# Kernel optimization log

Hardware: AMD Instinct MI355X
Metric: run time of the kernel (lower is better)

## Reference

```python
import jax, jax.numpy as jnp
import numpy as np

B, N, CIN, K = 4, 4096, 64, 16
MLP = [64, 64, 128]
EPS = 1e-5


def setup_inputs() -> dict:
    key = jax.random.key(0)
    ks = jax.random.split(key, 8)
    inp = {
        "xyz": jax.random.normal(ks[0], (B, N, 3), dtype=jnp.float32),
        "points": jax.random.normal(ks[1], (B, N, CIN), dtype=jnp.float32),
    }
    last = 3 + CIN
    for i, oc in enumerate(MLP):
        inp[f"w{i}"] = jax.random.normal(ks[2 + i], (oc, last), dtype=jnp.float32) * 0.05
        inp[f"b{i}"] = jnp.zeros((oc,), dtype=jnp.float32)
        inp[f"g{i}"] = jnp.ones((oc,), dtype=jnp.float32)
        inp[f"be{i}"] = jnp.zeros((oc,), dtype=jnp.float32)
        inp[f"rm{i}"] = jnp.zeros((oc,), dtype=jnp.float32)
        inp[f"rv{i}"] = jnp.ones((oc,), dtype=jnp.float32)
        last = oc
    return inp


def reference(xyz, points, w0, b0, g0, be0, rm0, rv0,
              w1, b1, g1, be1, rm1, rv1,
              w2, b2, g2, be2, rm2, rv2):
    # knn via squared pairwise distance (same argsort order as cdist)
    sq = jnp.sum(xyz * xyz, axis=-1)  # (B,N)
    d2 = sq[:, :, None] + sq[:, None, :] - 2.0 * jnp.einsum('bnc,bmc->bnm', xyz, xyz)
    _, idx = jax.lax.top_k(-d2, K)  # (B,N,K), smallest-distance neighbors

    bidx = jnp.arange(xyz.shape[0])[:, None, None]  # (B,1,1)
    grouped_xyz = xyz[bidx, idx] - xyz[:, :, None, :]     # (B,N,K,3) relative coords
    grouped_pts = points[bidx, idx]                        # (B,N,K,CIN)
    h = jnp.concatenate([grouped_xyz, grouped_pts], axis=-1)  # (B,N,K,3+CIN)

    layers = [(w0, b0, g0, be0, rm0, rv0),
              (w1, b1, g1, be1, rm1, rv1),
              (w2, b2, g2, be2, rm2, rv2)]
    for (w, b, g, be, rm, rv) in layers:
        # 1x1 conv == per-point linear; BN in eval mode (running stats)
        h = jnp.einsum('bnkc,oc->bnko', h, w) + b
        h = (h - rm) * jax.lax.rsqrt(rv + EPS) * g + be
        h = jax.nn.relu(h)
    new_points = jnp.max(h, axis=2)  # max over K neighbors -> (B,N,C_out)
    return new_points
```

## Files before the change

kernel.cpp:

```cpp
#include <hip/hip_runtime.h>

#define NPT   4096
#define KNN_K 16
#define EPSV  1e-5f

#define W1T_OFF 4352
#define B1_OFF  8448
#define W2T_OFF 8512
#define B2_OFF  16704
#define IDX_OFF 16832
#define P_OFF   344512
#define Q_OFF   1393088

typedef unsigned long long ull;

__device__ __forceinline__ ull minu64(ull a, ull b) { return a < b ? a : b; }
__device__ __forceinline__ ull maxu64(ull a, ull b) { return a > b ? a : b; }

__device__ __forceinline__ ull bitonic_sort64(ull v, int lane) {
#pragma unroll
  for (int k = 2; k <= 64; k <<= 1) {
#pragma unroll
    for (int j = k >> 1; j > 0; j >>= 1) {
      ull o = __shfl_xor(v, j);
      bool lower = (lane & j) == 0;
      bool up = (lane & k) == 0;
      v = (lower == up) ? minu64(v, o) : maxu64(v, o);
    }
  }
  return v;
}

__device__ __forceinline__ ull bitonic_merge64(ull v, int lane) {
#pragma unroll
  for (int j = 32; j > 0; j >>= 1) {
    ull o = __shfl_xor(v, j);
    v = ((lane & j) == 0) ? minu64(v, o) : maxu64(v, o);
  }
  return v;
}

__global__ __launch_bounds__(256) void mega_kernel(
    const float* __restrict__ xyz, const float* __restrict__ points,
    const float* __restrict__ w0, const float* __restrict__ b0, const float* __restrict__ g0,
    const float* __restrict__ be0, const float* __restrict__ rm0, const float* __restrict__ rv0,
    const float* __restrict__ w1, const float* __restrict__ b1, const float* __restrict__ g1,
    const float* __restrict__ be1, const float* __restrict__ rm1, const float* __restrict__ rv1,
    const float* __restrict__ w2, const float* __restrict__ b2, const float* __restrict__ g2,
    const float* __restrict__ be2, const float* __restrict__ rm2, const float* __restrict__ rv2,
    float* __restrict__ ws, int* __restrict__ knnOut) {
  __shared__ __align__(16) unsigned char smem[20480];
  int blk = blockIdx.x;
  int tid = threadIdx.x;

  if (blk < 4096) {
    float4* tile = (float4*)smem;
    ull* buf = (ull*)(smem + 16384);
    int lane = tid & 63, w = tid >> 6;
    int b = blk >> 10;
    int n = ((blk & 1023) << 2) + w;
    const float* xb = xyz + (size_t)b * NPT * 3;

    float4 q;
    {
      const float* qp = xb + n * 3;
      float qx = qp[0], qy = qp[1], qz = qp[2];
      float qsq = __fadd_rn(__fadd_rn(__fmul_rn(qx, qx), __fmul_rn(qy, qy)),
                            __fmul_rn(qz, qz));
      q = make_float4(qx, qy, qz, qsq);
    }
    ull R = ~0ull;
    ull thresh = ~0ull;
    int cnt = 0;
    ull ltmask = (lane == 0) ? 0ull : (~0ull >> (64 - lane));
    const float4* r4 = (const float4*)xb;

#pragma unroll 1
    for (int t = 0; t < 4; ++t) {
      __syncthreads();
      {
        int fo = 768 * t + 3 * tid;
        float4 A = r4[fo], B = r4[fo + 1], C = r4[fo + 2];
        float xs[4] = {A.x, A.w, B.z, C.y};
        float ys[4] = {A.y, B.x, B.w, C.z};
        float zs[4] = {A.z, B.y, C.x, C.w};
#pragma unroll
        for (int j = 0; j < 4; ++j) {
          float sq = __fadd_rn(__fadd_rn(__fmul_rn(xs[j], xs[j]), __fmul_rn(ys[j], ys[j])),
                               __fmul_rn(zs[j], zs[j]));
          tile[4 * tid + j] = make_float4(xs[j], ys[j], zs[j], sq);
        }
      }
      __syncthreads();
#pragma unroll 1
      for (int i = 0; i < 16; ++i) {
        int ml = (i << 6) + lane;
        float4 c = tile[ml];
        float dot = __fadd_rn(__fadd_rn(__fmul_rn(q.x, c.x), __fmul_rn(q.y, c.y)),
                              __fmul_rn(q.z, c.z));
        float d2 = __fsub_rn(__fadd_rn(q.w, c.w), __fmul_rn(2.0f, dot));
        unsigned bits = __float_as_uint(d2);
        unsigned fk = bits ^ (0x80000000u | (unsigned)((int)bits >> 31));
        ull key = ((ull)fk << 32) | (unsigned)((t << 10) + ml);
        bool pred = key < thresh;
        ull mask = __ballot(pred);
        if (mask) {
          int pos = cnt + __popcll(mask & ltmask);
          if (pred) buf[w * 128 + pos] = key;
          cnt += __popcll(mask);
          if (cnt >= 64) {
            ull v = buf[w * 128 + lane];
            v = bitonic_sort64(v, lane);
            ull vr = __shfl(v, 63 - lane);
            R = minu64(R, vr);
            R = bitonic_merge64(R, lane);
            thresh = __shfl(R, 15);
            cnt -= 64;
            if (lane < cnt) {
              ull tmp = buf[w * 128 + 64 + lane];
              buf[w * 128 + lane] = tmp;
            }
          }
        }
      }
    }
    {
      ull v = (lane < cnt) ? buf[w * 128 + lane] : ~0ull;
      v = bitonic_sort64(v, lane);
      ull vr = __shfl(v, 63 - lane);
      R = minu64(R, vr);
      R = bitonic_merge64(R, lane);
    }
    if (lane < KNN_K)
      knnOut[(b * NPT + n) * KNN_K + lane] = (int)(unsigned)(R & 0xFFFFFFFFull);
    return;
  }

  if (blk < 6144) {
    float* wlds = (float*)smem;
    for (int j = tid; j < 4288; j += 256) {
      int r = j / 67;
      float s = g0[r] * rsqrtf(rv0[r] + EPSV);
      wlds[j] = __fmul_rn(w0[j], s);
    }
    __syncthreads();
    int oc = tid & 63;
    int base = (blk - 4096) * 8 + (tid >> 6);
    float s = g0[oc] * rsqrtf(rv0[oc] + EPSV);
    float b0f = (b0[oc] - rm0[oc]) * s + be0[oc];
    const float* wrow = wlds + oc * 67;
#pragma unroll 1
    for (int pt = 0; pt < 2; ++pt) {
      int i = base + pt * 4;
      float x = xyz[i * 3], y = xyz[i * 3 + 1], z = xyz[i * 3 + 2];
      float qacc = wrow[0] * x;
      qacc = fmaf(wrow[1], y, qacc);
      qacc = fmaf(wrow[2], z, qacc);
      float acc = b0f + qacc;
      const float* prow = points + (size_t)i * 64;
#pragma unroll 4
      for (int c = 0; c < 64; ++c) acc = fmaf(wrow[3 + c], prow[c], acc);
      ws[P_OFF + (size_t)i * 64 + oc] = acc;
      ws[Q_OFF + (size_t)i * 64 + oc] = qacc;
    }
    return;
  }

  {
    int i = (blk - 6144) * 256 + tid + 4352;
    if (i < 8448) {
      int j = i - 4352; int oc = j & 63, ic = j >> 6;
      float s = g1[oc] * rsqrtf(rv1[oc] + EPSV);
      ws[i] = w1[oc * 64 + ic] * s;
    } else if (i < 8512) {
      int oc = i - 8448;
      float s = g1[oc] * rsqrtf(rv1[oc] + EPSV);
      ws[i] = (b1[oc] - rm1[oc]) * s + be1[oc];
    } else if (i < 16704) {
      int j = i - 8512; int ic = j >> 7, oc = j & 127;
      float s = g2[oc] * rsqrtf(rv2[oc] + EPSV);
      ws[i] = w2[oc * 64 + ic] * s;
    } else if (i < 16832) {
      int oc = i - 16704;
      float s = g2[oc] * rsqrtf(rv2[oc] + EPSV);
      ws[i] = (b2[oc] - rm2[oc]) * s + be2[oc];
    }
  }
}

__global__ __launch_bounds__(256, 4) void mlp_kernel(
    const float* __restrict__ wbuf, const int* __restrict__ knn,
    float* __restrict__ out) {
  __shared__ __align__(16) float Ash[64 * 128];
  __shared__ __align__(16) float Wsh[32 * 64];
  int tid = threadIdx.x;
  int qblk = blockIdx.x << 3;

  const float4* w1g = (const float4*)(wbuf + W1T_OFF);
  const float4* w2g = (const float4*)(wbuf + W2T_OFF);
  float4* wl = (float4*)Wsh;

#define W2IDX(e, p, h) ((((h) << 5) + ((e) >> 4)) * 32 + ((p) << 4) + ((e) & 15))

  float4 s0 = w1g[tid];
  float4 s1 = w1g[256 + tid];

  {
    int p = tid & 127, half = tid >> 7;
    int q = qblk + (p >> 4);
    int k = p & 15;
    int src = knn[q * KNN_K + k];
    int srow = (q & ~(NPT - 1)) + src;
    const float4* Pp = (const float4*)(wbuf + P_OFF + (size_t)srow * 64 + half * 32);
    const float4* Qp = (const float4*)(wbuf + Q_OFF + (size_t)q * 64 + half * 32);
#pragma unroll
    for (int j = 0; j < 8; ++j) {
      float4 pv = Pp[j];
      float4 qv = Qp[j];
      int ic = half * 32 + j * 4;
      Ash[(ic + 0) * 128 + p] = fmaxf(pv.x - qv.x, 0.0f);
      Ash[(ic + 1) * 128 + p] = fmaxf(pv.y - qv.y, 0.0f);
      Ash[(ic + 2) * 128 + p] = fmaxf(pv.z - qv.z, 0.0f);
      Ash[(ic + 3) * 128 + p] = fmaxf(pv.w - qv.w, 0.0f);
    }
  }
  wl[tid] = s0; wl[256 + tid] = s1;
  s0 = w1g[512 + tid]; s1 = w1g[768 + tid];
  __syncthreads();

  int og = tid & 7, pg = tid >> 3;
  const float* Arow = Ash + 4 * pg;
  const float* Wrow = Wsh + 8 * og;
  float acc[4][8];

#define GEMM32(R0)                                                        \
  _Pragma("unroll 8")                                                     \
  for (int ic = 0; ic < 32; ++ic) {                                       \
    float4 a0 = *(const float4*)(Arow + ((R0) + ic) * 128);               \
    float4 wv0 = *(const float4*)(Wrow + ic * 64);                        \
    float4 wv1 = *(const float4*)(Wrow + ic * 64 + 4);                    \
    float av[4] = {a0.x, a0.y, a0.z, a0.w};                               \
    float wv[8] = {wv0.x, wv0.y, wv0.z, wv0.w, wv1.x, wv1.y, wv1.z, wv1.w};\
    _Pragma("unroll")                                                     \
    for (int ii = 0; ii < 4; ++ii)                                        \
      _Pragma("unroll")                                                   \
      for (int jj = 0; jj < 8; ++jj) acc[ii][jj] = fmaf(av[ii], wv[jj], acc[ii][jj]); \
  }

  {
    float4 b0v = *(const float4*)(wbuf + B1_OFF + 8 * og);
    float4 b1v = *(const float4*)(wbuf + B1_OFF + 8 * og + 4);
    float bj[8] = {b0v.x, b0v.y, b0v.z, b0v.w, b1v.x, b1v.y, b1v.z, b1v.w};
#pragma unroll
    for (int i = 0; i < 4; ++i)
#pragma unroll
      for (int j = 0; j < 8; ++j) acc[i][j] = bj[j];
  }
  GEMM32(0)
  __syncthreads();
  wl[tid] = s0; wl[256 + tid] = s1;
  s0 = w2g[W2IDX(tid, 0, 0)]; s1 = w2g[W2IDX(tid + 256, 0, 0)];
  __syncthreads();
  GEMM32(32)
  __syncthreads();

#pragma unroll
  for (int j = 0; j < 8; ++j) {
    int oc = 8 * og + j;
    *(float4*)(Ash + oc * 128 + 4 * pg) =
        make_float4(fmaxf(acc[0][j], 0.0f), fmaxf(acc[1][j], 0.0f),
                    fmaxf(acc[2][j], 0.0f), fmaxf(acc[3][j], 0.0f));
  }
  wl[tid] = s0; wl[256 + tid] = s1;
  s0 = w2g[W2IDX(tid, 0, 1)]; s1 = w2g[W2IDX(tid + 256, 0, 1)];
  __syncthreads();

  int qout = qblk + (pg >> 2);
  float* obase = out + (size_t)qout * 128 + 8 * og;

  {
    float4 b0v = *(const float4*)(wbuf + B2_OFF + 8 * og);
    float4 b1v = *(const float4*)(wbuf + B2_OFF + 8 * og + 4);
    float bj[8] = {b0v.x, b0v.y, b0v.z, b0v.w, b1v.x, b1v.y, b1v.z, b1v.w};
#pragma unroll
    for (int i = 0; i < 4; ++i)
#pragma unroll
      for (int j = 0; j < 8; ++j) acc[i][j] = bj[j];
  }
  GEMM32(0)
  __syncthreads();
  wl[tid] = s0; wl[256 + tid] = s1;
  s0 = w2g[W2IDX(tid, 1, 0)]; s1 = w2g[W2IDX(tid + 256, 1, 0)];
  __syncthreads();
  GEMM32(32)
  {
    float m[8];
#pragma unroll
    for (int j = 0; j < 8; ++j) {
      float v = fmaxf(fmaxf(acc[0][j], acc[1][j]), fmaxf(acc[2][j], acc[3][j]));
      v = fmaxf(v, 0.0f);
      v = fmaxf(v, __shfl_xor(v, 8));
      m[j] = fmaxf(v, __shfl_xor(v, 16));
    }
    if ((pg & 3) == 0) {
      *(float4*)(obase)     = make_float4(m[0], m[1], m[2], m[3]);
      *(float4*)(obase + 4) = make_float4(m[4], m[5], m[6], m[7]);
    }
  }
  __syncthreads();
  wl[tid] = s0; wl[256 + tid] = s1;
  s0 = w2g[W2IDX(tid, 1, 1)]; s1 = w2g[W2IDX(tid + 256, 1, 1)];
  __syncthreads();

  {
    float4 b0v = *(const float4*)(wbuf + B2_OFF + 64 + 8 * og);
    float4 b1v = *(const float4*)(wbuf + B2_OFF + 64 + 8 * og + 4);
    float bj[8] = {b0v.x, b0v.y, b0v.z, b0v.w, b1v.x, b1v.y, b1v.z, b1v.w};
#pragma unroll
    for (int i = 0; i < 4; ++i)
#pragma unroll
      for (int j = 0; j < 8; ++j) acc[i][j] = bj[j];
  }
  GEMM32(0)
  __syncthreads();
  wl[tid] = s0; wl[256 + tid] = s1;
  __syncthreads();
  GEMM32(32)
  {
    float m[8];
#pragma unroll
    for (int j = 0; j < 8; ++j) {
      float v = fmaxf(fmaxf(acc[0][j], acc[1][j]), fmaxf(acc[2][j], acc[3][j]));
      v = fmaxf(v, 0.0f);
      v = fmaxf(v, __shfl_xor(v, 8));
      m[j] = fmaxf(v, __shfl_xor(v, 16));
    }
    if ((pg & 3) == 0) {
      *(float4*)(obase + 64)     = make_float4(m[0], m[1], m[2], m[3]);
      *(float4*)(obase + 64 + 4) = make_float4(m[4], m[5], m[6], m[7]);
    }
  }
#undef GEMM32
#undef W2IDX
}

extern "C" void kernel_launch(void* const* d_in, const int* in_sizes, int n_in,
                              void* d_out, int out_size, void* d_ws, size_t ws_size,
                              hipStream_t stream) {
  const float* xyz    = (const float*)d_in[0];
  const float* points = (const float*)d_in[1];
  float* wsF = (float*)d_ws;
  int* idxBuf = (int*)(wsF + IDX_OFF);

  mega_kernel<<<6193, 256, 0, stream>>>(
      xyz, points,
      (const float*)d_in[2],  (const float*)d_in[3],  (const float*)d_in[4],
      (const float*)d_in[5],  (const float*)d_in[6],  (const float*)d_in[7],
      (const float*)d_in[8],  (const float*)d_in[9],  (const float*)d_in[10],
      (const float*)d_in[11], (const float*)d_in[12], (const float*)d_in[13],
      (const float*)d_in[14], (const float*)d_in[15], (const float*)d_in[16],
      (const float*)d_in[17], (const float*)d_in[18], (const float*)d_in[19],
      wsF, idxBuf);
  mlp_kernel<<<2048, 256, 0, stream>>>(wsF, idxBuf, (float*)d_out);
}
```

Baseline: 259.8 us.

## Widen layer-2 MLP tile to 8x8 per thread and simplify kNN candidate filter

The final 64->128 layer now runs as one pass with an 8x8 register tile per thread covering all 128 output channels. It stages a 32x128 weight slab in shared memory instead of two separate 64-channel halves, which cuts weight reloads, barriers and one shuffle level in the max-reduction. In exchange, accumulators double and launch bounds drop to 3 blocks per CU. The kNN filter now compares only the 32-bit distance key against the threshold (using <=) and computes the compaction position with mbcnt, building the 64-bit key only for lanes that pass.

```diff
diff --git a/kernel.cpp b/kernel.cpp
--- a/kernel.cpp
+++ b/kernel.cpp
@@ -70,9 +70,8 @@
       q = make_float4(qx, qy, qz, qsq);
     }
     ull R = ~0ull;
-    ull thresh = ~0ull;
+    unsigned thresh_hi = 0xFFFFFFFFu;
     int cnt = 0;
-    ull ltmask = (lane == 0) ? 0ull : (~0ull >> (64 - lane));
     const float4* r4 = (const float4*)xb;
 
 #pragma unroll 1
@@ -94,19 +93,21 @@
       __syncthreads();
 #pragma unroll 1
       for (int i = 0; i < 16; ++i) {
-        int ml = (i << 6) + lane;
-        float4 c = tile[ml];
+        float4 c = tile[(i << 6) + lane];
         float dot = __fadd_rn(__fadd_rn(__fmul_rn(q.x, c.x), __fmul_rn(q.y, c.y)),
                               __fmul_rn(q.z, c.z));
         float d2 = __fsub_rn(__fadd_rn(q.w, c.w), __fmul_rn(2.0f, dot));
         unsigned bits = __float_as_uint(d2);
         unsigned fk = bits ^ (0x80000000u | (unsigned)((int)bits >> 31));
-        ull key = ((ull)fk << 32) | (unsigned)((t << 10) + ml);
-        bool pred = key < thresh;
+        bool pred = fk <= thresh_hi;
         ull mask = __ballot(pred);
         if (mask) {
-          int pos = cnt + __popcll(mask & ltmask);
-          if (pred) buf[w * 128 + pos] = key;
+          int pos = cnt + (int)__builtin_amdgcn_mbcnt_hi(
+                              (unsigned)(mask >> 32),
+                              __builtin_amdgcn_mbcnt_lo((unsigned)mask, 0u));
+          if (pred)
+            buf[w * 128 + pos] =
+                ((ull)fk << 32) | (unsigned)((t << 10) + (i << 6) + lane);
           cnt += __popcll(mask);
           if (cnt >= 64) {
             ull v = buf[w * 128 + lane];
@@ -114,7 +115,7 @@
             ull vr = __shfl(v, 63 - lane);
             R = minu64(R, vr);
             R = bitonic_merge64(R, lane);
-            thresh = __shfl(R, 15);
+            thresh_hi = (unsigned)__shfl((int)(unsigned)(R >> 32), 15);
             cnt -= 64;
             if (lane < cnt) {
               ull tmp = buf[w * 128 + 64 + lane];
@@ -188,11 +189,11 @@
   }
 }
 
-__global__ __launch_bounds__(256, 4) void mlp_kernel(
+__global__ __launch_bounds__(256, 3) void mlp_kernel(
     const float* __restrict__ wbuf, const int* __restrict__ knn,
     float* __restrict__ out) {
   __shared__ __align__(16) float Ash[64 * 128];
-  __shared__ __align__(16) float Wsh[32 * 64];
+  __shared__ __align__(16) float Wsh[32 * 128];
   int tid = threadIdx.x;
   int qblk = blockIdx.x << 3;
 
@@ -200,10 +201,11 @@
   const float4* w2g = (const float4*)(wbuf + W2T_OFF);
   float4* wl = (float4*)Wsh;
 
-#define W2IDX(e, p, h) ((((h) << 5) + ((e) >> 4)) * 32 + ((p) << 4) + ((e) & 15))
+#define W2C(e, h) ((((h) << 5) + ((e) >> 5)) * 32 + ((e) & 31))
 
   float4 s0 = w1g[tid];
   float4 s1 = w1g[256 + tid];
+  float4 s2, s3;
 
   {
     int p = tid & 127, half = tid >> 7;
@@ -231,7 +233,7 @@
   int og = tid & 7, pg = tid >> 3;
   const float* Arow = Ash + 4 * pg;
   const float* Wrow = Wsh + 8 * og;
-  float acc[4][8];
+  float acc[8][8];
 
 #define GEMM32(R0)                                                        \
   _Pragma("unroll 8")                                                     \
@@ -259,7 +261,8 @@
   GEMM32(0)
   __syncthreads();
   wl[tid] = s0; wl[256 + tid] = s1;
-  s0 = w2g[W2IDX(tid, 0, 0)]; s1 = w2g[W2IDX(tid + 256, 0, 0)];
+  s0 = w2g[W2C(tid, 0)];       s1 = w2g[W2C(tid + 256, 0)];
+  s2 = w2g[W2C(tid + 512, 0)]; s3 = w2g[W2C(tid + 768, 0)];
   __syncthreads();
   GEMM32(32)
   __syncthreads();
@@ -271,77 +274,64 @@
         make_float4(fmaxf(acc[0][j], 0.0f), fmaxf(acc[1][j], 0.0f),
                     fmaxf(acc[2][j], 0.0f), fmaxf(acc[3][j], 0.0f));
   }
-  wl[tid] = s0; wl[256 + tid] = s1;
-  s0 = w2g[W2IDX(tid, 0, 1)]; s1 = w2g[W2IDX(tid + 256, 0, 1)];
-  __syncthreads();
-
-  int qout = qblk + (pg >> 2);
-  float* obase = out + (size_t)qout * 128 + 8 * og;
-
-  {
-    float4 b0v = *(const float4*)(wbuf + B2_OFF + 8 * og);
-    float4 b1v = *(const float4*)(wbuf + B2_OFF + 8 * og + 4);
+  wl[tid] = s0; wl[256 + tid] = s1; wl[512 + tid] = s2; wl[768 + tid] = s3;
+  s0 = w2g[W2C(tid, 1)];       s1 = w2g[W2C(tid + 256, 1)];
+  s2 = w2g[W2C(tid + 512, 1)]; s3 = w2g[W2C(tid + 768, 1)];
+  __syncthreads();
+
+  int og2 = tid & 15, pg2 = tid >> 4;
+  const float* Arow2 = Ash + 8 * pg2;
+  const float* Wrow2 = Wsh + 8 * og2;
+
+#define GEMM32L2(R0)                                                      \
+  _Pragma("unroll 4")                                                     \
+  for (int ic = 0; ic < 32; ++ic) {                                       \
+    float4 a0 = *(const float4*)(Arow2 + ((R0) + ic) * 128);              \
+    float4 a1 = *(const float4*)(Arow2 + ((R0) + ic) * 128 + 4);          \
+    float4 wv0 = *(const float4*)(Wrow2 + ic * 128);                      \
+    float4 wv1 = *(const float4*)(Wrow2 + ic * 128 + 4);                  \
+    float av[8] = {a0.x, a0.y, a0.z, a0.w, a1.x, a1.y, a1.z, a1.w};       \
+    float wv[8] = {wv0.x, wv0.y, wv0.z, wv0.w, wv1.x, wv1.y, wv1.z, wv1.w};\
+    _Pragma("unroll")                                                     \
+    for (int ii = 0; ii < 8; ++ii)                                        \
+      _Pragma("unroll")                                                   \
+      for (int jj = 0; jj < 8; ++jj) acc[ii][jj] = fmaf(av[ii], wv[jj], acc[ii][jj]); \
+  }
+
+  {
+    float4 b0v = *(const float4*)(wbuf + B2_OFF + 8 * og2);
+    float4 b1v = *(const float4*)(wbuf + B2_OFF + 8 * og2 + 4);
     float bj[8] = {b0v.x, b0v.y, b0v.z, b0v.w, b1v.x, b1v.y, b1v.z, b1v.w};
 #pragma unroll
-    for (int i = 0; i < 4; ++i)
+    for (int i = 0; i < 8; ++i)
 #pragma unroll
       for (int j = 0; j < 8; ++j) acc[i][j] = bj[j];
   }
-  GEMM32(0)
-  __syncthreads();
-  wl[tid] = s0; wl[256 + tid] = s1;
-  s0 = w2g[W2IDX(tid, 1, 0)]; s1 = w2g[W2IDX(tid + 256, 1, 0)];
-  __syncthreads();
-  GEMM32(32)
-  {
+  GEMM32L2(0)
+  __syncthreads();
+  wl[tid] = s0; wl[256 + tid] = s1; wl[512 + tid] = s2; wl[768 + tid] = s3;
+  __syncthreads();
+  GEMM32L2(32)
+
+  {
+    int qout = qblk + (pg2 >> 1);
+    float* obase = out + (size_t)qout * 128 + 8 * og2;
     float m[8];
 #pragma unroll
     for (int j = 0; j < 8; ++j) {
-      float v = fmaxf(fmaxf(acc[0][j], acc[1][j]), fmaxf(acc[2][j], acc[3][j]));
+      float v = fmaxf(fmaxf(fmaxf(acc[0][j], acc[1][j]), fmaxf(acc[2][j], acc[3][j])),
+                      fmaxf(fmaxf(acc[4][j], acc[5][j]), fmaxf(acc[6][j], acc[7][j])));
       v = fmaxf(v, 0.0f);
-      v = fmaxf(v, __shfl_xor(v, 8));
       m[j] = fmaxf(v, __shfl_xor(v, 16));
     }
-    if ((pg & 3) == 0) {
+    if ((pg2 & 1) == 0) {
       *(float4*)(obase)     = make_float4(m[0], m[1], m[2], m[3]);
       *(float4*)(obase + 4) = make_float4(m[4], m[5], m[6], m[7]);
     }
   }
-  __syncthreads();
-  wl[tid] = s0; wl[256 + tid] = s1;
-  s0 = w2g[W2IDX(tid, 1, 1)]; s1 = w2g[W2IDX(tid + 256, 1, 1)];
-  __syncthreads();
-
-  {
-    float4 b0v = *(const float4*)(wbuf + B2_OFF + 64 + 8 * og);
-    float4 b1v = *(const float4*)(wbuf + B2_OFF + 64 + 8 * og + 4);
-    float bj[8] = {b0v.x, b0v.y, b0v.z, b0v.w, b1v.x, b1v.y, b1v.z, b1v.w};
-#pragma unroll
-    for (int i = 0; i < 4; ++i)
-#pragma unroll
-      for (int j = 0; j < 8; ++j) acc[i][j] = bj[j];
-  }
-  GEMM32(0)
-  __syncthreads();
-  wl[tid] = s0; wl[256 + tid] = s1;
-  __syncthreads();
-  GEMM32(32)
-  {
-    float m[8];
-#pragma unroll
-    for (int j = 0; j < 8; ++j) {
-      float v = fmaxf(fmaxf(acc[0][j], acc[1][j]), fmaxf(acc[2][j], acc[3][j]));
-      v = fmaxf(v, 0.0f);
-      v = fmaxf(v, __shfl_xor(v, 8));
-      m[j] = fmaxf(v, __shfl_xor(v, 16));
-    }
-    if ((pg & 3) == 0) {
-      *(float4*)(obase + 64)     = make_float4(m[0], m[1], m[2], m[3]);
-      *(float4*)(obase + 64 + 4) = make_float4(m[4], m[5], m[6], m[7]);
-    }
-  }
 #undef GEMM32
-#undef W2IDX
+#undef GEMM32L2
+#undef W2C
 }
 
 extern "C" void kernel_launch(void* const* d_in, const int* in_sizes, int n_in,
```

Result: no change. 260.6 us (+0.3%).
